# Kernel optimization log

Measured on AMD Instinct MI355X. Metric: run time of the kernel, lower is better.

## Reference

```python
import jax, jax.numpy as jnp
import numpy as np

RADIUS = 0.1
NSAMPLE = 32
EPS = 1e-5


def ball_query(p, radius, k):
    # p: (B,N,3) -> idx: (B,N,k) int32. For each query point, take the first k
    # points (in index order) within `radius`; pad with the first found index.
    B, N, _ = p.shape
    d2 = jnp.sum((p[:, :, None, :] - p[:, None, :, :]) ** 2, axis=-1)  # (B,N,N)
    j = jnp.arange(N, dtype=jnp.int32)
    key = jnp.where(d2 < radius * radius, j[None, None, :], N)  # invalid -> N
    neg_small, _ = jax.lax.top_k(-key, k)  # k smallest keys, ascending
    idx = -neg_small                        # (B,N,k)
    first = idx[..., :1]
    idx = jnp.where(idx == N, first, idx)   # pad missing neighbors with first
    return idx


def conv_bn_relu(f, W, g, b, relu=True):
    # f: (B,Cin,N,K); W: (Cout,Cin) 1x1 conv; BatchNorm2d (training stats) + ReLU
    y = jnp.einsum('oc,bcnk->bonk', W, f)
    mean = jnp.mean(y, axis=(0, 2, 3), keepdims=True)
    var = jnp.var(y, axis=(0, 2, 3), keepdims=True)
    y = (y - mean) * jax.lax.rsqrt(var + EPS)
    y = y * g[None, :, None, None] + b[None, :, None, None]
    return jax.nn.relu(y) if relu else y


def reference(p, x, W1, g1, b1, W2, g2, b2):
    # p: (B,N,3), x: (B,C,N)
    B, N, _ = p.shape
    idx = ball_query(p, RADIUS, NSAMPLE)                    # (B,N,K)
    pj = jax.vmap(lambda pts, ix: pts[ix])(p, idx)          # (B,N,K,3)
    dp = pj - p[:, :, None, :]                              # relative coords
    dp = jnp.transpose(dp, (0, 3, 1, 2))                    # (B,3,N,K)
    xt = jnp.transpose(x, (0, 2, 1))                        # (B,N,C)
    xj = jax.vmap(lambda ft, ix: ft[ix])(xt, idx)           # (B,N,K,C)
    xj = jnp.transpose(xj, (0, 3, 1, 2))                    # (B,C,N,K)
    f = jnp.concatenate([dp, xj], axis=1)                   # (B,3+C,N,K)
    f = conv_bn_relu(f, W1, g1, b1, relu=True)
    f = conv_bn_relu(f, W2, g2, b2, relu=True)              # last_act=True
    return jnp.max(f, axis=-1)                              # (B,Cout,N)


def setup_inputs() -> dict:
    key = jax.random.key(0)
    ks = jax.random.split(key, 4)
    B, N, C = 4, 4096, 32
    Cin, Cout = 3 + C, 64
    return {
        'p': jax.random.uniform(ks[0], (B, N, 3), dtype=jnp.float32),
        'x': jax.random.normal(ks[1], (B, C, N), dtype=jnp.float32),
        'W1': jax.random.normal(ks[2], (Cout, Cin), dtype=jnp.float32) * 0.1,
        'g1': jnp.ones((Cout,), jnp.float32),
        'b1': jnp.zeros((Cout,), jnp.float32),
        'W2': jax.random.normal(ks[3], (Cout, Cout), dtype=jnp.float32) * 0.1,
        'g2': jnp.ones((Cout,), jnp.float32),
        'b2': jnp.zeros((Cout,), jnp.float32),
    }
```

## Files before the change

kernel.cpp:

```cpp
#include <hip/hip_runtime.h>
#include <stdint.h>


#define R2 0.01f
#define INVM (1.0f / 524288.0f)

typedef __bf16 bf16x8 __attribute__((ext_vector_type(8)));
typedef float f32x4 __attribute__((ext_vector_type(4)));

__device__ __forceinline__ uint32_t pack_bf16(float a, float b) {
  uint32_t ua = __float_as_uint(a), ub = __float_as_uint(b);
  ua += 0x7fffu + ((ua >> 16) & 1u);
  ub += 0x7fffu + ((ub >> 16) & 1u);
  return (ua >> 16) | (ub & 0xffff0000u);
}

__device__ __forceinline__ int cell_of(float v) {
  const int c = (int)(v * 10.f);
  return c > 9 ? 9 : c;
}

__global__ __launch_bounds__(1024) void k_front(const float* __restrict__ p,
                                                const float* __restrict__ x,
                                                const float* __restrict__ W1,
                                                const float* __restrict__ W2,
                                                float* __restrict__ u,
                                                float* __restrict__ q,
                                                uint32_t* __restrict__ w2frag,
                                                float* __restrict__ part1b,
                                                float* __restrict__ part2b,
                                                float4* __restrict__ cellpts,
                                                int* __restrict__ cellStart) {
  __shared__ __align__(16) char smraw[61440];
  const int bid = blockIdx.x, tid = threadIdx.x;

  if (bid < 128) {
    float* W1s = (float*)smraw;
    for (int tt = tid; tt < 2240; tt += 1024) {
      const int o = tt / 35, cc = tt - o * 35;
      W1s[(cc << 6) + o] = W1[tt];
    }
    __syncthreads();
    const int t = tid & 255, sb = tid >> 8;
    const int g = (bid << 7) + (sb << 5) + (t & 31);
    const int b = g >> 12, nl = g & 4095;
    const int os = (t >> 5) << 3;
    float f[35];
    const float* pb = p + g * 3;
    f[0] = pb[0]; f[1] = pb[1]; f[2] = pb[2];
    const float* xb = x + (b << 17) + nl;
#pragma unroll
    for (int cc = 0; cc < 32; ++cc) f[3 + cc] = xb[cc << 12];
    float acc[8];
#pragma unroll
    for (int o = 0; o < 8; ++o) acc[o] = 0.f;
#pragma unroll
    for (int cc = 0; cc < 35; ++cc) {
      const float fc = f[cc];
      const float4* wp = (const float4*)(W1s + (cc << 6) + os);
      const float4 w0 = wp[0], w1 = wp[1];
      acc[0] = fmaf(w0.x, fc, acc[0]); acc[1] = fmaf(w0.y, fc, acc[1]);
      acc[2] = fmaf(w0.z, fc, acc[2]); acc[3] = fmaf(w0.w, fc, acc[3]);
      acc[4] = fmaf(w1.x, fc, acc[4]); acc[5] = fmaf(w1.y, fc, acc[5]);
      acc[6] = fmaf(w1.z, fc, acc[6]); acc[7] = fmaf(w1.w, fc, acc[7]);
      if (cc == 2) {
        *(float4*)(q + (g << 6) + os)     = make_float4(acc[0], acc[1], acc[2], acc[3]);
        *(float4*)(q + (g << 6) + os + 4) = make_float4(acc[4], acc[5], acc[6], acc[7]);
      }
    }
    *(float4*)(u + (g << 6) + os)     = make_float4(acc[0], acc[1], acc[2], acc[3]);
    *(float4*)(u + (g << 6) + os + 4) = make_float4(acc[4], acc[5], acc[6], acc[7]);
    return;
  }

  if (bid == 128) {
    for (int tt = tid; tt < 2048; tt += 1024) {
      const int e2 = tt & 3, lane = (tt >> 2) & 63, frag = tt >> 8;
      const int kt = frag >> 2, ot = frag & 3;
      const int c0 = kt * 32 + ((lane >> 4) << 3) + e2 * 2;
      const int o = ot * 16 + (lane & 15);
      w2frag[tt] = pack_bf16(W2[(o << 6) + c0], W2[(o << 6) + c0 + 1]);
    }
    part1b[tid] = 0.f;
    part2b[tid] = 0.f;
    return;
  }

  float* px = (float*)smraw;
  float* py = px + 4096;
  float* pz = py + 4096;
  int* cnt_s = (int*)(smraw + 49152);
  int* scanA = (int*)(smraw + 53248);
  int* scanB = (int*)(smraw + 57344);
  const int b = bid - 129;
  const float* pb = p + b * 12288;
  cnt_s[tid] = 0;
  for (int i = tid; i < 4096; i += 1024) {
    px[i] = pb[3 * i]; py[i] = pb[3 * i + 1]; pz[i] = pb[3 * i + 2];
  }
  __syncthreads();
  for (int i = tid; i < 4096; i += 1024) {
    const int c = (cell_of(px[i]) * 10 + cell_of(py[i])) * 10 + cell_of(pz[i]);
    atomicAdd(&cnt_s[c], 1);
  }
  __syncthreads();
  int* src = scanA; int* dst = scanB;
  src[tid] = cnt_s[tid];
  __syncthreads();
  for (int d = 1; d < 1024; d <<= 1) {
    int v = src[tid];
    if (tid >= d) v += src[tid - d];
    dst[tid] = v;
    __syncthreads();
    int* tmp = src; src = dst; dst = tmp;
  }
  const int excl = (tid == 0) ? 0 : src[tid - 1];
  if (tid <= 1000) cellStart[b * 1001 + tid] = (tid < 1000) ? excl : src[999];
  cnt_s[tid] = excl;
  __syncthreads();
  for (int i = tid; i < 4096; i += 1024) {
    const float xx = px[i], yy = py[i], zz = pz[i];
    const int c = (cell_of(xx) * 10 + cell_of(yy)) * 10 + cell_of(zz);
    const int pos = atomicAdd(&cnt_s[c], 1);
    cellpts[(b << 12) + pos] = make_float4(xx, yy, zz, __int_as_float(i));
  }
}

__global__ __launch_bounds__(512) void k_query(const float* __restrict__ p,
                                               const float4* __restrict__ cellpts,
                                               const int* __restrict__ cellStart,
                                               int* __restrict__ idx) {
  __shared__ float ps[24];
  __shared__ uint32_t bm[8][128];
  const int tid = threadIdx.x, w = tid >> 6, lane = tid & 63;
  const int blk0 = blockIdx.x;
  const int blkS = ((blk0 & 7) << 8) + (blk0 >> 3);
  const int p0 = blkS << 3;
  const int b = p0 >> 12;
  const int n = p0 + w;
  if (tid < 24) ps[tid] = p[p0 * 3 + tid];
  bm[w][lane] = 0; bm[w][64 + lane] = 0;
  __syncthreads();
  const float qx = ps[w * 3], qy = ps[w * 3 + 1], qz = ps[w * 3 + 2];
  const int cxq = cell_of(qx), cyq = cell_of(qy), czq = cell_of(qz);

  int cnt_l = 0, startG = 0;
  if (lane < 27) {
    const int cx = cxq + lane / 9 - 1;
    const int cy = cyq + (lane / 3) % 3 - 1;
    const int cz = czq + lane % 3 - 1;
    if ((unsigned)cx < 10u && (unsigned)cy < 10u && (unsigned)cz < 10u) {
      const int* cs = cellStart + b * 1001 + (cx * 10 + cy) * 10 + cz;
      startG = cs[0];
      cnt_l = cs[1] - startG;
    }
  }
  int incl = cnt_l;
#pragma unroll
  for (int d = 1; d < 64; d <<= 1) { const int t = __shfl_up(incl, d); if (lane >= d) incl += t; }
  const int T = __shfl(incl, 63);
  const int base_l = startG - (incl - cnt_l);

  for (int tb = 0; tb < T; tb += 64) {
    const int t = tb + lane;
    int s = 0;
#pragma unroll
    for (int m = 0; m < 27; ++m) s += (__shfl(incl, m) <= t);
    const int a = __shfl(base_l, s < 27 ? s : 26);
    if (t < T) {
      const float4 cp = cellpts[(b << 12) + a + t];
      const float dx = cp.x - qx, dy = cp.y - qy, dz = cp.z - qz;
      const float d2 = __fadd_rn(__fadd_rn(__fmul_rn(dx, dx), __fmul_rn(dy, dy)),
                                 __fmul_rn(dz, dz));
      if (d2 < R2) {
        const int j = __float_as_int(cp.w);
        atomicOr(&bm[w][j >> 5], 1u << (j & 31));
      }
    }
  }
  __threadfence_block();

  const uint2 wp2 = *(const uint2*)&bm[w][2 * lane];
  unsigned long long wd = ((unsigned long long)wp2.y << 32) | wp2.x;
  const int pc = __popcll(wd);
  int ip = pc;
#pragma unroll
  for (int d = 1; d < 64; d <<= 1) { const int t = __shfl_up(ip, d); if (lane >= d) ip += t; }
  const int cntT = __shfl(ip, 63);
  int bpos = ip - pc;
  const unsigned long long nz = __ballot(wd != 0ull);
  const int fl = (int)__builtin_ctzll(nz);
  const int fv = wd ? ((lane << 6) + (int)__builtin_ctzll(wd)) : 0;
  const int first = __shfl(fv, fl);
  int* row = idx + (n << 5);
  unsigned long long ww = wd;
  while (ww && bpos < 32) {
    const int j = (lane << 6) + (int)__builtin_ctzll(ww);
    row[bpos] = j;
    ++bpos;
    ww &= ww - 1;
  }
  for (int s = cntT + lane; s < 32; s += 64) row[s] = first;
}

__global__ __launch_bounds__(256) void k_bn1(const float* __restrict__ u,
                                             const float* __restrict__ q,
                                             const int* __restrict__ idx,
                                             float* __restrict__ part1b) {
  __shared__ int idxs[512];
  __shared__ __align__(16) float qs[1024];
  __shared__ float red[8][64];
  const int tid = threadIdx.x;
  const int blk0 = blockIdx.x;
  const int blkS = ((blk0 & 7) << 7) + (blk0 >> 3);
  const int p0 = blkS << 4;
  const int bb = (p0 >> 12) << 12;
  idxs[tid] = idx[(p0 << 5) + tid];
  idxs[256 + tid] = idx[(p0 << 5) + 256 + tid];
#pragma unroll
  for (int i = 0; i < 4; ++i) qs[(i << 8) + tid] = q[(p0 << 6) + (i << 8) + tid];
  __syncthreads();
  const int c = tid & 3;
  float s1[16], s2[16];
#pragma unroll
  for (int i = 0; i < 16; ++i) { s1[i] = 0.f; s2[i] = 0.f; }
#pragma unroll 2
  for (int pass = 0; pass < 8; ++pass) {
    const int r = (pass << 6) + (tid >> 2);
    const int j = idxs[r];
    const int pt = r >> 5;
    const float* up = u + ((bb + j) << 6) + (c << 2);
    const float* qp = qs + (pt << 6) + (c << 2);
#pragma unroll
    for (int i = 0; i < 4; ++i) {
      const float4 uv = *(const float4*)(up + (i << 4));
      const float4 qv = *(const float4*)(qp + (i << 4));
      const float y0 = uv.x - qv.x, y1 = uv.y - qv.y;
      const float y2 = uv.z - qv.z, y3 = uv.w - qv.w;
      s1[4 * i + 0] += y0; s2[4 * i + 0] = fmaf(y0, y0, s2[4 * i + 0]);
      s1[4 * i + 1] += y1; s2[4 * i + 1] = fmaf(y1, y1, s2[4 * i + 1]);
      s1[4 * i + 2] += y2; s2[4 * i + 2] = fmaf(y2, y2, s2[4 * i + 2]);
      s1[4 * i + 3] += y3; s2[4 * i + 3] = fmaf(y3, y3, s2[4 * i + 3]);
    }
  }
#pragma unroll
  for (int i = 0; i < 16; ++i) {
#pragma unroll
    for (int d = 4; d <= 32; d <<= 1) {
      s1[i] += __shfl_xor(s1[i], d);
      s2[i] += __shfl_xor(s2[i], d);
    }
  }
  const int w = tid >> 6, l = tid & 63;
  if (l < 4) {
#pragma unroll
    for (int i = 0; i < 16; ++i) {
      const int ch = ((i >> 2) << 4) + (l << 2) + (i & 3);
      red[(w << 1)][ch] = s1[i];
      red[(w << 1) + 1][ch] = s2[i];
    }
  }
  __syncthreads();
  if (tid < 128) {
    const int ch = tid & 63, stat = tid >> 6;
    const float v = red[stat][ch] + red[2 + stat][ch] + red[4 + stat][ch] + red[6 + stat][ch];
    atomicAdd(&part1b[((blk0 & 7) << 7) + (stat << 6) + ch], v);
  }
}

__global__ __launch_bounds__(256) void k_stage2(const float* __restrict__ u,
                                                const int* __restrict__ idx,
                                                const float* __restrict__ q,
                                                const float* __restrict__ part1b,
                                                const float* __restrict__ g1,
                                                const float* __restrict__ b1,
                                                const uint32_t* __restrict__ w2frag,
                                                float* __restrict__ part2b,
                                                float* __restrict__ ymax,
                                                float* __restrict__ ymin) {
  __shared__ uint32_t hl[8192];
  __shared__ float rs[8][64];
  __shared__ int   idxs[256];
  __shared__ float ac[128];
  __shared__ float red[8][64];
  const int tid = threadIdx.x, w = tid >> 6, l = tid & 63;
  const int blk0 = blockIdx.x;
  const int blk = ((blk0 & 7) << 8) + (blk0 >> 3);
  const int p0 = blk << 3;
  const int bb = (p0 >> 12) << 12;

  idxs[tid] = idx[(p0 << 5) + tid];
  const float qa = q[(p0 << 6) + tid];
  const float qb = q[(p0 << 6) + 256 + tid];
  if (tid < 64) {
    float s1 = 0.f, s2 = 0.f;
#pragma unroll
    for (int xx = 0; xx < 8; ++xx) {
      s1 += part1b[(xx << 7) + tid];
      s2 += part1b[(xx << 7) + 64 + tid];
    }
    const float mean = s1 * INVM, var = s2 * INVM - mean * mean;
    const float a = g1[tid] * rsqrtf(var + 1e-5f);
    ac[tid] = a; ac[64 + tid] = b1[tid] - mean * a;
  }
  __syncthreads();
  rs[tid >> 6][tid & 63] = fmaf(-ac[tid & 63], qa, ac[64 + (tid & 63)]);
  rs[4 + (tid >> 6)][tid & 63] = fmaf(-ac[tid & 63], qb, ac[64 + (tid & 63)]);
  __syncthreads();

  const int c = tid & 3;
#pragma unroll
  for (int pass = 0; pass < 4; ++pass) {
    const int r = (pass << 6) + (tid >> 2);
    const int pt = r >> 5;
    const int j = idxs[r];
    const float* up = u + ((bb + j) << 6);
    float4 uv[4];
#pragma unroll
    for (int i = 0; i < 4; ++i) uv[i] = *(const float4*)(up + (i << 4) + (c << 2));
#pragma unroll
    for (int i = 0; i < 4; ++i) {
      const int ch0 = (i << 4) + (c << 2);
      const f32x4 a = *(const f32x4*)&ac[ch0];
      const f32x4 rv = *(const f32x4*)&rs[pt][ch0];
      const float h0 = fmaxf(fmaf(a[0], uv[i].x, rv[0]), 0.f);
      const float h1 = fmaxf(fmaf(a[1], uv[i].y, rv[1]), 0.f);
      const float h2 = fmaxf(fmaf(a[2], uv[i].z, rv[2]), 0.f);
      const float h3 = fmaxf(fmaf(a[3], uv[i].w, rv[3]), 0.f);
      int byte = (r << 7) + (ch0 << 1);
      byte ^= (r & 7) << 4;
      *(uint2*)((char*)hl + byte) = make_uint2(pack_bf16(h0, h1), pack_bf16(h2, h3));
    }
  }

  bf16x8 bfr[8];
#pragma unroll
  for (int f = 0; f < 8; ++f)
    bfr[f] = __builtin_bit_cast(bf16x8, *(const uint4*)&w2frag[(f << 8) + (l << 2)]);
  __syncthreads();

  float sm_[4] = {0.f, 0.f, 0.f, 0.f}, sq[4] = {0.f, 0.f, 0.f, 0.f};
#pragma unroll 1
  for (int pi = 0; pi < 2; ++pi) {
    const int ptl = (w << 1) + pi;
    const int pn = p0 + ptl;
    float mx[4], mn[4];
#pragma unroll
    for (int ot = 0; ot < 4; ++ot) { mx[ot] = -3e38f; mn[ot] = 3e38f; }
#pragma unroll
    for (int kt2 = 0; kt2 < 2; ++kt2) {
      bf16x8 afr[2];
#pragma unroll
      for (int kt = 0; kt < 2; ++kt) {
        const int srow = (ptl << 5) + (kt2 << 4) + (l & 15);
        int byte = (srow << 7) + (kt << 6) + ((l >> 4) << 4);
        byte ^= (srow & 7) << 4;
        afr[kt] = *(const bf16x8*)((const char*)hl + byte);
      }
#pragma unroll
      for (int ot = 0; ot < 4; ++ot) {
        f32x4 acc = {0.f, 0.f, 0.f, 0.f};
        acc = __builtin_amdgcn_mfma_f32_16x16x32_bf16(afr[0], bfr[ot], acc, 0, 0, 0);
        acc = __builtin_amdgcn_mfma_f32_16x16x32_bf16(afr[1], bfr[4 + ot], acc, 0, 0, 0);
#pragma unroll
        for (int e = 0; e < 4; ++e) {
          const float v = acc[e];
          mx[ot] = fmaxf(mx[ot], v); mn[ot] = fminf(mn[ot], v);
          sm_[ot] += v; sq[ot] = fmaf(v, v, sq[ot]);
        }
      }
    }
#pragma unroll
    for (int ot = 0; ot < 4; ++ot) {
      float a = fmaxf(mx[ot], __shfl_xor(mx[ot], 16)); a = fmaxf(a, __shfl_xor(a, 32));
      float b = fminf(mn[ot], __shfl_xor(mn[ot], 16)); b = fminf(b, __shfl_xor(b, 32));
      const int o = (ot << 4) + (l & 15);
      if (l < 16)      ymax[(pn << 6) + o] = a;
      else if (l < 32) ymin[(pn << 6) + o] = b;
    }
  }
#pragma unroll
  for (int ot = 0; ot < 4; ++ot) {
    float s = sm_[ot]; s += __shfl_xor(s, 16); s += __shfl_xor(s, 32);
    float t2 = sq[ot]; t2 += __shfl_xor(t2, 16); t2 += __shfl_xor(t2, 32);
    if (l < 16) { red[w][(ot << 4) + l] = s; red[4 + w][(ot << 4) + l] = t2; }
  }
  __syncthreads();
  if (tid < 128) {
    const int ch = tid & 63, sel = (tid >= 64) ? 4 : 0;
    const float v = red[sel][ch] + red[sel + 1][ch] + red[sel + 2][ch] + red[sel + 3][ch];
    atomicAdd(&part2b[((blk0 & 7) << 7) + tid], v);
  }
}

__global__ __launch_bounds__(256) void k_out(const float* __restrict__ ymax,
                                             const float* __restrict__ ymin,
                                             const float* __restrict__ part2b,
                                             const float* __restrict__ g2,
                                             const float* __restrict__ b2,
                                             float* __restrict__ out) {
  __shared__ float ac[128];
  __shared__ float tile[64][65];
  const int tid = threadIdx.x;
  if (tid < 64) {
    float s1 = 0.f, s2 = 0.f;
#pragma unroll
    for (int xx = 0; xx < 8; ++xx) {
      s1 += part2b[(xx << 7) + tid];
      s2 += part2b[(xx << 7) + 64 + tid];
    }
    const float mean = s1 * INVM, var = s2 * INVM - mean * mean;
    const float a = g2[tid] * rsqrtf(var + 1e-5f);
    ac[tid] = a; ac[64 + tid] = b2[tid] - mean * a;
  }
  __syncthreads();
  const int b = blockIdx.x >> 6, nt = blockIdx.x & 63;
  const int pnbase = (b << 12) + (nt << 6);
#pragma unroll
  for (int i = 0; i < 16; ++i) {
    const int e = i * 256 + tid;
    const int nl = e >> 6, o = e & 63;
    const float a = ac[o], c = ac[64 + o];
    const int src = ((pnbase + nl) << 6) + o;
    const float v = (a >= 0.f) ? ymax[src] : ymin[src];
    tile[nl][o] = fmaxf(fmaf(a, v, c), 0.f);
  }
  __syncthreads();
#pragma unroll
  for (int i = 0; i < 16; ++i) {
    const int e = i * 256 + tid;
    const int ol = e >> 6, nl = e & 63;
    out[(b << 18) + (ol << 12) + (nt << 6) + nl] = tile[nl][ol];
  }
}

extern "C" void kernel_launch(void* const* d_in, const int* in_sizes, int n_in,
                              void* d_out, int out_size, void* d_ws, size_t ws_size,
                              hipStream_t stream) {
  const float* p  = (const float*)d_in[0];
  const float* x  = (const float*)d_in[1];
  const float* W1 = (const float*)d_in[2];
  const float* g1 = (const float*)d_in[3];
  const float* b1 = (const float*)d_in[4];
  const float* W2 = (const float*)d_in[5];
  const float* g2 = (const float*)d_in[6];
  const float* b2 = (const float*)d_in[7];
  float* out = (float*)d_out;

  char* ws = (char*)d_ws;
  size_t off = 0;
  int* idx        = (int*)(ws + off);      off += 2097152;
  float* u        = (float*)(ws + off);    off += 4194304;
  float* q        = (float*)(ws + off);    off += 4194304;
  uint32_t* w2f   = (uint32_t*)(ws + off); off += 8192;
  float* part1b   = (float*)(ws + off);    off += 4096;
  float* part2b   = (float*)(ws + off);    off += 4096;
  float* ymax     = (float*)(ws + off);    off += 4194304;
  float* ymin     = (float*)(ws + off);    off += 4194304;
  float4* cellpts = (float4*)(ws + off);   off += 262144;
  int* cellStart  = (int*)(ws + off);      off += 16384;

  k_front<<<dim3(133), dim3(1024), 0, stream>>>(p, x, W1, W2, u, q, w2f,
                                                part1b, part2b, cellpts, cellStart);
  k_query<<<dim3(2048), dim3(512), 0, stream>>>(p, cellpts, cellStart, idx);
  k_bn1<<<dim3(1024), dim3(256), 0, stream>>>(u, q, idx, part1b);
  k_stage2<<<dim3(2048), dim3(256), 0, stream>>>(u, idx, q, part1b, g1, b1, w2f,
                                                 part2b, ymax, ymin);
  k_out<<<dim3(256), dim3(256), 0, stream>>>(ymax, ymin, part2b, g2, b2, out);
}
```

Measured before the change: 62.58 us.

## Store gathered conv1 output in bf16 and merge z-adjacent cells in ball query

The per-point conv1 output u is now packed to bf16, which halves its size and the gather traffic in the BN1 statistics and stage-2 kernels. Both consumers are rewritten to read contiguous 32-byte chunks per thread and unpack them, and stage 2 writes its swizzled LDS rows with 16-byte stores. The ball query now treats the three z-adjacent cells as one contiguous range, since cells are sorted with z fastest, so it scans 9 ranges instead of 27. It also uses 4-wave blocks that read query coordinates directly, without a shared-memory sync. Rounding u to bf16 before the batch-norm statistics adds error relative to the fp32 path.

```diff
diff --git a/kernel.cpp b/kernel.cpp
--- a/kernel.cpp
+++ b/kernel.cpp
@@ -14,6 +14,8 @@
   ub += 0x7fffu + ((ub >> 16) & 1u);
   return (ua >> 16) | (ub & 0xffff0000u);
 }
+__device__ __forceinline__ float bf_lo(uint32_t v) { return __uint_as_float(v << 16); }
+__device__ __forceinline__ float bf_hi(uint32_t v) { return __uint_as_float(v & 0xffff0000u); }
 
 __device__ __forceinline__ int cell_of(float v) {
   const int c = (int)(v * 10.f);
@@ -24,7 +26,7 @@
                                                 const float* __restrict__ x,
                                                 const float* __restrict__ W1,
                                                 const float* __restrict__ W2,
-                                                float* __restrict__ u,
+                                                void* __restrict__ u,
                                                 float* __restrict__ q,
                                                 uint32_t* __restrict__ w2frag,
                                                 float* __restrict__ part1b,
@@ -68,8 +70,12 @@
         *(float4*)(q + (g << 6) + os + 4) = make_float4(acc[4], acc[5], acc[6], acc[7]);
       }
     }
-    *(float4*)(u + (g << 6) + os)     = make_float4(acc[0], acc[1], acc[2], acc[3]);
-    *(float4*)(u + (g << 6) + os + 4) = make_float4(acc[4], acc[5], acc[6], acc[7]);
+    uint4 pk;
+    pk.x = pack_bf16(acc[0], acc[1]);
+    pk.y = pack_bf16(acc[2], acc[3]);
+    pk.z = pack_bf16(acc[4], acc[5]);
+    pk.w = pack_bf16(acc[6], acc[7]);
+    *(uint4*)((char*)u + ((size_t)g << 7) + (os << 1)) = pk;
     return;
   }
 
@@ -126,33 +132,30 @@
   }
 }
 
-__global__ __launch_bounds__(512) void k_query(const float* __restrict__ p,
+__global__ __launch_bounds__(256) void k_query(const float* __restrict__ p,
                                                const float4* __restrict__ cellpts,
                                                const int* __restrict__ cellStart,
                                                int* __restrict__ idx) {
-  __shared__ float ps[24];
-  __shared__ uint32_t bm[8][128];
+  __shared__ uint32_t bm[4][128];
   const int tid = threadIdx.x, w = tid >> 6, lane = tid & 63;
   const int blk0 = blockIdx.x;
-  const int blkS = ((blk0 & 7) << 8) + (blk0 >> 3);
-  const int p0 = blkS << 3;
-  const int b = p0 >> 12;
-  const int n = p0 + w;
-  if (tid < 24) ps[tid] = p[p0 * 3 + tid];
+  const int blkS = ((blk0 & 7) << 9) + (blk0 >> 3);
+  const int n = (blkS << 2) + w;
+  const int b = n >> 12;
   bm[w][lane] = 0; bm[w][64 + lane] = 0;
-  __syncthreads();
-  const float qx = ps[w * 3], qy = ps[w * 3 + 1], qz = ps[w * 3 + 2];
+  const float qx = p[n * 3], qy = p[n * 3 + 1], qz = p[n * 3 + 2];
   const int cxq = cell_of(qx), cyq = cell_of(qy), czq = cell_of(qz);
 
   int cnt_l = 0, startG = 0;
-  if (lane < 27) {
-    const int cx = cxq + lane / 9 - 1;
-    const int cy = cyq + (lane / 3) % 3 - 1;
-    const int cz = czq + lane % 3 - 1;
-    if ((unsigned)cx < 10u && (unsigned)cy < 10u && (unsigned)cz < 10u) {
-      const int* cs = cellStart + b * 1001 + (cx * 10 + cy) * 10 + cz;
-      startG = cs[0];
-      cnt_l = cs[1] - startG;
+  if (lane < 9) {
+    const int cx = cxq + lane / 3 - 1;
+    const int cy = cyq + lane % 3 - 1;
+    if ((unsigned)cx < 10u && (unsigned)cy < 10u) {
+      const int zlo = czq > 0 ? czq - 1 : 0;
+      const int zhi = czq < 9 ? czq + 1 : 9;
+      const int* cs = cellStart + b * 1001 + (cx * 10 + cy) * 10;
+      startG = cs[zlo];
+      cnt_l = cs[zhi + 1] - startG;
     }
   }
   int incl = cnt_l;
@@ -165,8 +168,8 @@
     const int t = tb + lane;
     int s = 0;
 #pragma unroll
-    for (int m = 0; m < 27; ++m) s += (__shfl(incl, m) <= t);
-    const int a = __shfl(base_l, s < 27 ? s : 26);
+    for (int m = 0; m < 9; ++m) s += (__shfl(incl, m) <= t);
+    const int a = __shfl(base_l, s < 9 ? s : 8);
     if (t < T) {
       const float4 cp = cellpts[(b << 12) + a + t];
       const float dx = cp.x - qx, dy = cp.y - qy, dz = cp.z - qz;
@@ -203,7 +206,7 @@
   for (int s = cntT + lane; s < 32; s += 64) row[s] = first;
 }
 
-__global__ __launch_bounds__(256) void k_bn1(const float* __restrict__ u,
+__global__ __launch_bounds__(256) void k_bn1(const void* __restrict__ u,
                                              const float* __restrict__ q,
                                              const int* __restrict__ idx,
                                              float* __restrict__ part1b) {
@@ -220,7 +223,8 @@
 #pragma unroll
   for (int i = 0; i < 4; ++i) qs[(i << 8) + tid] = q[(p0 << 6) + (i << 8) + tid];
   __syncthreads();
-  const int c = tid & 3;
+  const int c4 = tid & 3;
+  const char* ub = (const char*)u;
   float s1[16], s2[16];
 #pragma unroll
   for (int i = 0; i < 16; ++i) { s1[i] = 0.f; s2[i] = 0.f; }
@@ -229,18 +233,16 @@
     const int r = (pass << 6) + (tid >> 2);
     const int j = idxs[r];
     const int pt = r >> 5;
-    const float* up = u + ((bb + j) << 6) + (c << 2);
-    const float* qp = qs + (pt << 6) + (c << 2);
-#pragma unroll
-    for (int i = 0; i < 4; ++i) {
-      const float4 uv = *(const float4*)(up + (i << 4));
-      const float4 qv = *(const float4*)(qp + (i << 4));
-      const float y0 = uv.x - qv.x, y1 = uv.y - qv.y;
-      const float y2 = uv.z - qv.z, y3 = uv.w - qv.w;
-      s1[4 * i + 0] += y0; s2[4 * i + 0] = fmaf(y0, y0, s2[4 * i + 0]);
-      s1[4 * i + 1] += y1; s2[4 * i + 1] = fmaf(y1, y1, s2[4 * i + 1]);
-      s1[4 * i + 2] += y2; s2[4 * i + 2] = fmaf(y2, y2, s2[4 * i + 2]);
-      s1[4 * i + 3] += y3; s2[4 * i + 3] = fmaf(y3, y3, s2[4 * i + 3]);
+    const uint4* up = (const uint4*)(ub + ((size_t)(bb + j) << 7) + (c4 << 5));
+    const uint4 u0 = up[0], u1 = up[1];
+    const float* qp = qs + (pt << 6) + (c4 << 4);
+    const uint32_t uw[8] = {u0.x, u0.y, u0.z, u0.w, u1.x, u1.y, u1.z, u1.w};
+#pragma unroll
+    for (int e = 0; e < 8; ++e) {
+      const float y0 = bf_lo(uw[e]) - qp[2 * e];
+      const float y1 = bf_hi(uw[e]) - qp[2 * e + 1];
+      s1[2 * e] += y0;     s2[2 * e] = fmaf(y0, y0, s2[2 * e]);
+      s1[2 * e + 1] += y1; s2[2 * e + 1] = fmaf(y1, y1, s2[2 * e + 1]);
     }
   }
 #pragma unroll
@@ -255,7 +257,7 @@
   if (l < 4) {
 #pragma unroll
     for (int i = 0; i < 16; ++i) {
-      const int ch = ((i >> 2) << 4) + (l << 2) + (i & 3);
+      const int ch = (l << 4) + i;
       red[(w << 1)][ch] = s1[i];
       red[(w << 1) + 1][ch] = s2[i];
     }
@@ -268,7 +270,7 @@
   }
 }
 
-__global__ __launch_bounds__(256) void k_stage2(const float* __restrict__ u,
+__global__ __launch_bounds__(256) void k_stage2(const void* __restrict__ u,
                                                 const int* __restrict__ idx,
                                                 const float* __restrict__ q,
                                                 const float* __restrict__ part1b,
@@ -309,28 +311,33 @@
   __syncthreads();
 
   const int c = tid & 3;
+  const char* ub = (const char*)u;
+  f32x4 av[4];
+#pragma unroll
+  for (int k = 0; k < 4; ++k) av[k] = *(const f32x4*)&ac[(c << 4) + (k << 2)];
 #pragma unroll
   for (int pass = 0; pass < 4; ++pass) {
     const int r = (pass << 6) + (tid >> 2);
     const int pt = r >> 5;
     const int j = idxs[r];
-    const float* up = u + ((bb + j) << 6);
-    float4 uv[4];
-#pragma unroll
-    for (int i = 0; i < 4; ++i) uv[i] = *(const float4*)(up + (i << 4) + (c << 2));
-#pragma unroll
-    for (int i = 0; i < 4; ++i) {
-      const int ch0 = (i << 4) + (c << 2);
-      const f32x4 a = *(const f32x4*)&ac[ch0];
-      const f32x4 rv = *(const f32x4*)&rs[pt][ch0];
-      const float h0 = fmaxf(fmaf(a[0], uv[i].x, rv[0]), 0.f);
-      const float h1 = fmaxf(fmaf(a[1], uv[i].y, rv[1]), 0.f);
-      const float h2 = fmaxf(fmaf(a[2], uv[i].z, rv[2]), 0.f);
-      const float h3 = fmaxf(fmaf(a[3], uv[i].w, rv[3]), 0.f);
-      int byte = (r << 7) + (ch0 << 1);
-      byte ^= (r & 7) << 4;
-      *(uint2*)((char*)hl + byte) = make_uint2(pack_bf16(h0, h1), pack_bf16(h2, h3));
-    }
+    const uint4* up = (const uint4*)(ub + ((size_t)(bb + j) << 7) + (c << 5));
+    const uint4 u0 = up[0], u1 = up[1];
+    f32x4 rv4[4];
+#pragma unroll
+    for (int k = 0; k < 4; ++k) rv4[k] = *(const f32x4*)&rs[pt][(c << 4) + (k << 2)];
+    const uint32_t uw[8] = {u0.x, u0.y, u0.z, u0.w, u1.x, u1.y, u1.z, u1.w};
+    uint32_t pk[8];
+#pragma unroll
+    for (int e = 0; e < 8; ++e) {
+      const int i0 = 2 * e, i1 = 2 * e + 1;
+      const float h0 = fmaxf(fmaf(av[i0 >> 2][i0 & 3], bf_lo(uw[e]), rv4[i0 >> 2][i0 & 3]), 0.f);
+      const float h1 = fmaxf(fmaf(av[i1 >> 2][i1 & 3], bf_hi(uw[e]), rv4[i1 >> 2][i1 & 3]), 0.f);
+      pk[e] = pack_bf16(h0, h1);
+    }
+    const int byte0 = (r << 7) + (c << 5);
+    const int sw = (r & 7) << 4;
+    *(uint4*)((char*)hl + (byte0 ^ sw)) = make_uint4(pk[0], pk[1], pk[2], pk[3]);
+    *(uint4*)((char*)hl + ((byte0 + 16) ^ sw)) = make_uint4(pk[4], pk[5], pk[6], pk[7]);
   }
 
   bf16x8 bfr[8];
@@ -450,7 +457,7 @@
   char* ws = (char*)d_ws;
   size_t off = 0;
   int* idx        = (int*)(ws + off);      off += 2097152;
-  float* u        = (float*)(ws + off);    off += 4194304;
+  void* u         = (void*)(ws + off);     off += 2097152;
   float* q        = (float*)(ws + off);    off += 4194304;
   uint32_t* w2f   = (uint32_t*)(ws + off); off += 8192;
   float* part1b   = (float*)(ws + off);    off += 4096;
@@ -462,7 +469,7 @@
 
   k_front<<<dim3(133), dim3(1024), 0, stream>>>(p, x, W1, W2, u, q, w2f,
                                                 part1b, part2b, cellpts, cellStart);
-  k_query<<<dim3(2048), dim3(512), 0, stream>>>(p, cellpts, cellStart, idx);
+  k_query<<<dim3(4096), dim3(256), 0, stream>>>(p, cellpts, cellStart, idx);
   k_bn1<<<dim3(1024), dim3(256), 0, stream>>>(u, q, idx, part1b);
   k_stage2<<<dim3(2048), dim3(256), 0, stream>>>(u, idx, q, part1b, g1, b1, w2f,
                                                  part2b, ymax, ymin);
```

Result: faster. 54.73 us (-12.5%).
